# Kernel optimization log

Hardware: AMD Instinct MI355X
Metric: run time of the kernel (lower is better)

The kernel has to match this reference:

```python
import jax, jax.numpy as jnp
import numpy as np

B, T, C, H = 4, 2048, 1024, 16
HS = C // H  # head_size = 64


def setup_inputs() -> dict:
    key = jax.random.key(0)
    ks = jax.random.split(key, 12)
    s_in = C ** -0.5
    s_ff = (4 * C) ** -0.5
    return {
        "x": jax.random.normal(ks[0], (B, T, C), jnp.float32),
        "Wq": jax.random.normal(ks[1], (H, C, HS), jnp.float32) * s_in,
        "Wk": jax.random.normal(ks[2], (H, C, HS), jnp.float32) * s_in,
        "Wv": jax.random.normal(ks[3], (H, C, HS), jnp.float32) * s_in,
        "Wp": jax.random.normal(ks[4], (C, C), jnp.float32) * s_in,
        "bp": jnp.zeros((C,), jnp.float32),
        "W1": jax.random.normal(ks[5], (C, 4 * C), jnp.float32) * s_in,
        "b1": jnp.zeros((4 * C,), jnp.float32),
        "W2": jax.random.normal(ks[6], (4 * C, C), jnp.float32) * s_ff,
        "b2": jnp.zeros((C,), jnp.float32),
        "g1": jnp.ones((C,), jnp.float32),
        "be1": jnp.zeros((C,), jnp.float32),
        "g2": jnp.ones((C,), jnp.float32),
        "be2": jnp.zeros((C,), jnp.float32),
    }


def _layernorm(x, g, b, eps=1e-5):
    mu = jnp.mean(x, axis=-1, keepdims=True)
    var = jnp.var(x, axis=-1, keepdims=True)
    return (x - mu) * jax.lax.rsqrt(var + eps) * g + b


def reference(x, Wq, Wk, Wv, Wp, bp, W1, b1, W2, b2, g1, be1, g2, be2):
    # NOTE: residuals add to the post-LN tensor (faithful to the torch code),
    # and the attention scale uses C = n_embed, not head_size.
    x1 = _layernorm(x, g1, be1)                       # [B,T,C]
    q = jnp.einsum('btc,hcd->bhtd', x1, Wq)
    k = jnp.einsum('btc,hcd->bhtd', x1, Wk)
    v = jnp.einsum('btc,hcd->bhtd', x1, Wv)
    scores = jnp.einsum('bhtd,bhsd->bhts', q, k) * (C ** -0.5)
    causal = jnp.tril(jnp.ones((T, T), bool))
    scores = jnp.where(causal, scores, -jnp.inf)
    att = jax.nn.softmax(scores, axis=-1)             # [B,H,T,T]
    o = jnp.einsum('bhts,bhsd->bhtd', att, v)
    o = o.transpose(0, 2, 1, 3).reshape(B, T, C)      # concat heads
    x2 = x1 + o @ Wp + bp
    x3 = _layernorm(x2, g2, be2)
    ff = jax.nn.relu(x3 @ W1 + b1) @ W2 + b2
    return x3 + ff
```

## Files before the change

### kernel.cpp

```cpp
#include <hip/hip_runtime.h>
#include <cstdint>

typedef unsigned short u16;
typedef unsigned int u32;
typedef __bf16 bf16x8 __attribute__((ext_vector_type(8)));
typedef float f32x4 __attribute__((ext_vector_type(4)));

#define DEVINL __device__ __forceinline__

DEVINL float bf2f(u16 h) { union { u32 u; float f; } v; v.u = ((u32)h) << 16; return v.f; }
DEVINL u16 f2bf(float f) {
  union { __bf16 h; u16 u; } v;
  v.h = (__bf16)f;
  return v.u;
}

DEVINL float fexp2(float x) {
#if __has_builtin(__builtin_amdgcn_exp2f)
  return __builtin_amdgcn_exp2f(x);
#else
  return exp2f(x);
#endif
}

DEVINL void gld_lds16(const void* g, void* l) {
  __builtin_amdgcn_global_load_lds(
      (__attribute__((address_space(1))) void*)(g),
      (__attribute__((address_space(3))) void*)(l), 16, 0, 0);
}

__global__ __launch_bounds__(256) void kprep(
    const float* __restrict__ x, const float* __restrict__ Wq,
    const float* __restrict__ Wk, const float* __restrict__ Wv,
    const float* __restrict__ Wp, const float* __restrict__ W1,
    const float* __restrict__ W2, const float* __restrict__ g,
    const float* __restrict__ be, u16* __restrict__ x1,
    u16* __restrict__ wqkvT, u16* __restrict__ wpT,
    u16* __restrict__ w1T, u16* __restrict__ w2T) {
  int b = blockIdx.x;
  int t = threadIdx.x;
  if (b < 8192) {
    long row = b;
    float4 xv = *(const float4*)&x[row * 1024 + t * 4];
    float f0 = xv.x, f1 = xv.y, f2 = xv.z, f3 = xv.w;
    float s = f0 + f1 + f2 + f3;
    float s2 = f0 * f0 + f1 * f1 + f2 * f2 + f3 * f3;
#pragma unroll
    for (int off = 32; off >= 1; off >>= 1) {
      s += __shfl_xor(s, off);
      s2 += __shfl_xor(s2, off);
    }
    __shared__ float red[8];
    int w = t >> 6, l = t & 63;
    if (l == 0) { red[w] = s; red[4 + w] = s2; }
    __syncthreads();
    s = red[0] + red[1] + red[2] + red[3];
    s2 = red[4] + red[5] + red[6] + red[7];
    float mu = s * (1.0f / 1024.0f);
    float var = s2 * (1.0f / 1024.0f) - mu * mu;
    float rs = rsqrtf(var + 1e-5f);
    float4 gv = *(const float4*)&g[t * 4];
    float4 bv = *(const float4*)&be[t * 4];
    ushort4 ov;
    ov.x = f2bf((f0 - mu) * rs * gv.x + bv.x);
    ov.y = f2bf((f1 - mu) * rs * gv.y + bv.y);
    ov.z = f2bf((f2 - mu) * rs * gv.z + bv.z);
    ov.w = f2bf((f3 - mu) * rs * gv.w + bv.w);
    *(ushort4*)&x1[row * 1024 + t * 4] = ov;
    return;
  }
  int jb = b - 8192;
  const float* in;
  u16* out;
  int R, C, c0, r0;
  if (jb < 768) {
    int which = jb >> 8;
    int idx = jb & 255;
    int z = idx >> 4, y = idx & 15;
    const float* W = (which == 0) ? Wq : ((which == 1) ? Wk : Wv);
    in = W + (long)z * 65536;
    out = wqkvT + (long)which * 1048576 + (long)z * 65536;
    R = 1024; C = 64; c0 = 0; r0 = y * 64;
  } else if (jb < 1024) {
    int idx = jb - 768;
    in = Wp; out = wpT; R = 1024; C = 1024;
    c0 = (idx & 15) * 64; r0 = (idx >> 4) * 64;
  } else if (jb < 2048) {
    int idx = jb - 1024;
    in = W1; out = w1T; R = 1024; C = 4096;
    c0 = (idx & 63) * 64; r0 = (idx >> 6) * 64;
  } else {
    int idx = jb - 2048;
    in = W2; out = w2T; R = 4096; C = 1024;
    c0 = (idx & 15) * 64; r0 = (idx >> 4) * 64;
  }
  __shared__ __align__(16) u16 tile[64][80];
#pragma unroll
  for (int ph = 0; ph < 2; ++ph) {
    int ch = ph * 256 + t;
    int r = ch >> 3, cc = (ch & 7) * 8;
    const float* src = &in[(long)(r0 + r) * C + c0 + cc];
    float4 a = *(const float4*)src;
    float4 bb = *(const float4*)(src + 4);
    u16 tmp[8] = {f2bf(a.x), f2bf(a.y), f2bf(a.z), f2bf(a.w),
                  f2bf(bb.x), f2bf(bb.y), f2bf(bb.z), f2bf(bb.w)};
    *(uint4*)&tile[r][cc] = *(uint4*)tmp;
  }
  __syncthreads();
#pragma unroll
  for (int ph = 0; ph < 2; ++ph) {
    int ch = ph * 256 + t;
    int c = ch >> 3, rr = (ch & 7) * 8;
    u16 tmp[8];
#pragma unroll
    for (int i = 0; i < 8; ++i) tmp[i] = tile[rr + i][c];
    *(uint4*)&out[(long)(c0 + c) * R + r0 + rr] = *(uint4*)tmp;
  }
}

__global__ __launch_bounds__(256) void kln_b(const u16* __restrict__ x,
                                             const float* __restrict__ g,
                                             const float* __restrict__ be,
                                             u16* __restrict__ y) {
  long row = blockIdx.x;
  int t = threadIdx.x;
  ushort4 xv = *(const ushort4*)&x[row * 1024 + t * 4];
  float f0 = bf2f(xv.x), f1 = bf2f(xv.y), f2 = bf2f(xv.z), f3 = bf2f(xv.w);
  float s = f0 + f1 + f2 + f3;
  float s2 = f0 * f0 + f1 * f1 + f2 * f2 + f3 * f3;
#pragma unroll
  for (int off = 32; off >= 1; off >>= 1) {
    s += __shfl_xor(s, off);
    s2 += __shfl_xor(s2, off);
  }
  __shared__ float red[8];
  int w = t >> 6, l = t & 63;
  if (l == 0) { red[w] = s; red[4 + w] = s2; }
  __syncthreads();
  s = red[0] + red[1] + red[2] + red[3];
  s2 = red[4] + red[5] + red[6] + red[7];
  float mu = s * (1.0f / 1024.0f);
  float var = s2 * (1.0f / 1024.0f) - mu * mu;
  float rs = rsqrtf(var + 1e-5f);
  float4 gv = *(const float4*)&g[t * 4];
  float4 bv = *(const float4*)&be[t * 4];
  ushort4 ov;
  ov.x = f2bf((f0 - mu) * rs * gv.x + bv.x);
  ov.y = f2bf((f1 - mu) * rs * gv.y + bv.y);
  ov.z = f2bf((f2 - mu) * rs * gv.z + bv.z);
  ov.w = f2bf((f3 - mu) * rs * gv.w + bv.w);
  *(ushort4*)&y[row * 1024 + t * 4] = ov;
}

template <int EPI, int OF32>
__global__ __launch_bounds__(256) void kgemm(const u16* __restrict__ A,
                                             const u16* __restrict__ BT, int K,
                                             const float* __restrict__ bias,
                                             const u16* __restrict__ resid,
                                             void* __restrict__ outv, int ldc,
                                             u16* __restrict__ vout) {
  __shared__ __align__(16) u16 sA[128 * 64];
  __shared__ __align__(16) u16 sB[128 * 64];
  int tid = threadIdx.x;
  int l = tid & 63, wv = tid >> 6;
  int wm = (wv >> 1) * 64, wn = (wv & 1) * 64;
  int flat = blockIdx.y * gridDim.x + blockIdx.x;
  int cpx = (gridDim.x * gridDim.y) >> 3;
  int lg = (flat & 7) * cpx + (flat >> 3);
  int bx = lg % gridDim.x, by = lg / gridDim.x;
  long m0 = (long)by * 128, n0 = (long)bx * 128;
  const u16* Ab = A + m0 * K;
  const u16* Bb = BT + n0 * K;
  f32x4 acc[4][4] = {};

  for (int k0 = 0; k0 < K; k0 += 64) {
    __syncthreads();
#pragma unroll
    for (int it = 0; it < 4; ++it) {
      int c = it * 256 + tid;
      int r = c >> 3;
      int k8 = (c & 7) ^ (r & 7);
      gld_lds16(Ab + (long)r * K + k0 + k8 * 8, &sA[c * 8]);
    }
#pragma unroll
    for (int it = 0; it < 4; ++it) {
      int c = it * 256 + tid;
      int r = c >> 3;
      int k8 = (c & 7) ^ (r & 7);
      gld_lds16(Bb + (long)r * K + k0 + k8 * 8, &sB[c * 8]);
    }
    __syncthreads();
#pragma unroll
    for (int kk = 0; kk < 2; ++kk) {
      int k8 = kk * 4 + (l >> 4);
      bf16x8 af[4], bfr[4];
#pragma unroll
      for (int mi = 0; mi < 4; ++mi) {
        int r = wm + mi * 16 + (l & 15);
        af[mi] = *(const bf16x8*)&sA[(r * 8 + (k8 ^ (r & 7))) * 8];
      }
#pragma unroll
      for (int ni = 0; ni < 4; ++ni) {
        int r = wn + ni * 16 + (l & 15);
        bfr[ni] = *(const bf16x8*)&sB[(r * 8 + (k8 ^ (r & 7))) * 8];
      }
#pragma unroll
      for (int mi = 0; mi < 4; ++mi)
#pragma unroll
        for (int ni = 0; ni < 4; ++ni)
          acc[mi][ni] =
              __builtin_amdgcn_mfma_f32_16x16x32_bf16(af[mi], bfr[ni], acc[mi][ni], 0, 0, 0);
    }
  }
#pragma unroll
  for (int mi = 0; mi < 4; ++mi) {
#pragma unroll
    for (int ni = 0; ni < 4; ++ni) {
#pragma unroll
      for (int j = 0; j < 4; ++j) {
        long row = m0 + wm + mi * 16 + (l >> 4) * 4 + j;
        long col = n0 + wn + ni * 16 + (l & 15);
        float v = acc[mi][ni][j];
        if constexpr (EPI == 0) {
          long tn = col >> 10, jj = col & 1023;
          long hh = jj >> 6, dd = jj & 63;
          long bb = row >> 11, tt = row & 2047;
          if (tn == 0) {
            v *= 0.045084220027780106f;
            ((u16*)outv)[(((bb)*16 + hh) * 2048 + tt) * 64 + dd] = f2bf(v);
          } else if (tn == 1) {
            ((u16*)outv)[(((4 + bb) * 16 + hh) * 2048 + tt) * 64 + dd] = f2bf(v);
          } else {
            vout[((bb * 16 + hh) * 64 + dd) * 2048 + tt] = f2bf(v);
          }
        } else {
          v += bias[col];
          if constexpr (EPI == 2) v = fmaxf(v, 0.0f);
          if constexpr (EPI == 1) v += bf2f(resid[row * ldc + col]);
          if constexpr (OF32) ((float*)outv)[row * ldc + col] = v;
          else ((u16*)outv)[row * ldc + col] = f2bf(v);
        }
      }
    }
  }
}

__global__ __launch_bounds__(256) void kattn(const u16* __restrict__ q,
                                             const u16* __restrict__ kmat,
                                             const u16* __restrict__ vt,
                                             u16* __restrict__ o) {
  __shared__ __align__(16) u16 Ks[64 * 64];
  __shared__ __align__(16) u16 Vs[64 * 64];
  __shared__ __align__(16) u16 Ps[4 * 32 * 64];
  int bh = blockIdx.x;
  int qi = (gridDim.y - 1) - blockIdx.y;
  int tid = threadIdx.x, w = tid >> 6, l = tid & 63;
  long bQ = (long)bh * 2048 * 64;
  int qrow0 = qi * 128 + w * 32;
  const float NEGINF = -__builtin_inff();

  bf16x8 qf[2][2];
#pragma unroll
  for (int mi = 0; mi < 2; ++mi)
#pragma unroll
    for (int kk = 0; kk < 2; ++kk) {
      int tt = qrow0 + mi * 16 + (l & 15);
      int kd = kk * 32 + (l >> 4) * 8;
      qf[mi][kk] = *(const bf16x8*)&q[bQ + (long)tt * 64 + kd];
    }
  f32x4 ao[2][4] = {};
  float mr[2] = {NEGINF, NEGINF}, lr[2] = {0.f, 0.f};

  u16* Pw = &Ps[w * 2048];
  int g = l >> 4;
  int njt = qi * 2 + 2;
  for (int jt = 0; jt < njt; ++jt) {
    int s0 = jt * 64;
    bool skip = (s0 > qrow0 + 31);
    bool need_mask = (s0 + 63 > qrow0);
    __syncthreads();
#pragma unroll
    for (int it = 0; it < 2; ++it) {
      int c = it * 256 + tid;
      int r = c >> 3;
      int k8 = (c & 7) ^ (r & 7);
      gld_lds16(&kmat[bQ + (long)(s0 + r) * 64 + k8 * 8], &Ks[c * 8]);
    }
#pragma unroll
    for (int it = 0; it < 2; ++it) {
      int c = it * 256 + tid;
      int r = c >> 3;
      int s8 = (c & 7) ^ (r & 7);
      gld_lds16(&vt[bQ + (long)r * 2048 + s0 + s8 * 8], &Vs[c * 8]);
    }
    __syncthreads();
    if (skip) continue;
    f32x4 sc[2][4] = {};
#pragma unroll
    for (int kk = 0; kk < 2; ++kk) {
      int k8 = kk * 4 + g;
      bf16x8 kf[4];
#pragma unroll
      for (int ni = 0; ni < 4; ++ni) {
        int r = ni * 16 + (l & 15);
        kf[ni] = *(const bf16x8*)&Ks[(r * 8 + (k8 ^ (r & 7))) * 8];
      }
#pragma unroll
      for (int mi = 0; mi < 2; ++mi)
#pragma unroll
        for (int ni = 0; ni < 4; ++ni)
          sc[mi][ni] =
              __builtin_amdgcn_mfma_f32_16x16x32_bf16(kf[ni], qf[mi][kk], sc[mi][ni], 0, 0, 0);
    }
#pragma unroll
    for (int mi = 0; mi < 2; ++mi) {
      float rmax = NEGINF;
      if (need_mask) {
        int tg = qrow0 + mi * 16 + (l & 15);
#pragma unroll
        for (int ni = 0; ni < 4; ++ni)
#pragma unroll
          for (int j = 0; j < 4; ++j) {
            int sg = s0 + ni * 16 + g * 4 + j;
            float vv = sc[mi][ni][j];
            vv = (sg <= tg) ? vv : NEGINF;
            sc[mi][ni][j] = vv;
            rmax = fmaxf(rmax, vv);
          }
      } else {
#pragma unroll
        for (int ni = 0; ni < 4; ++ni)
#pragma unroll
          for (int j = 0; j < 4; ++j) rmax = fmaxf(rmax, sc[mi][ni][j]);
      }
      rmax = fmaxf(rmax, __shfl_xor(rmax, 16));
      rmax = fmaxf(rmax, __shfl_xor(rmax, 32));
      if (!__all(rmax <= mr[mi] + 11.5f)) {
        float mnew = fmaxf(mr[mi], rmax);
        float alpha = fexp2(mr[mi] - mnew);
        mr[mi] = mnew;
        lr[mi] *= alpha;
#pragma unroll
        for (int j = 0; j < 4; ++j) {
          float at = __shfl(alpha, g * 4 + j);
#pragma unroll
          for (int nd = 0; nd < 4; ++nd) ao[mi][nd][j] *= at;
        }
      }
      float rsum = 0.f;
#pragma unroll
      for (int ni = 0; ni < 4; ++ni)
#pragma unroll
        for (int j = 0; j < 4; ++j) {
          float p = fexp2(sc[mi][ni][j] - mr[mi]);
          sc[mi][ni][j] = p;
          rsum += p;
        }
      rsum += __shfl_xor(rsum, 16);
      rsum += __shfl_xor(rsum, 32);
      lr[mi] += rsum;
    }
#pragma unroll
    for (int mi = 0; mi < 2; ++mi) {
      int r = mi * 16 + (l & 15);
#pragma unroll
      for (int ni = 0; ni < 4; ++ni) {
        int cc0 = ni * 16 + g * 4;
        int addr = (r * 8 + ((cc0 >> 3) ^ (r & 7))) * 8 + (cc0 & 7);
        u16 h4[4] = {f2bf(sc[mi][ni][0]), f2bf(sc[mi][ni][1]),
                     f2bf(sc[mi][ni][2]), f2bf(sc[mi][ni][3])};
        *(uint2*)&Pw[addr] = *(uint2*)h4;
      }
    }
#pragma unroll
    for (int kk = 0; kk < 2; ++kk) {
      int s8 = kk * 4 + g;
      bf16x8 pf[2], vf[4];
#pragma unroll
      for (int mi = 0; mi < 2; ++mi) {
        int r = mi * 16 + (l & 15);
        pf[mi] = *(const bf16x8*)&Pw[(r * 8 + (s8 ^ (r & 7))) * 8];
      }
#pragma unroll
      for (int nd = 0; nd < 4; ++nd) {
        int r = nd * 16 + (l & 15);
        vf[nd] = *(const bf16x8*)&Vs[(r * 8 + (s8 ^ (r & 7))) * 8];
      }
#pragma unroll
      for (int mi = 0; mi < 2; ++mi)
#pragma unroll
        for (int nd = 0; nd < 4; ++nd)
          ao[mi][nd] =
              __builtin_amdgcn_mfma_f32_16x16x32_bf16(pf[mi], vf[nd], ao[mi][nd], 0, 0, 0);
    }
  }
  int b = bh >> 4, h = bh & 15;
#pragma unroll
  for (int mi = 0; mi < 2; ++mi) {
#pragma unroll
    for (int j = 0; j < 4; ++j) {
      float lrt = __shfl(lr[mi], g * 4 + j);
      float rinv = 1.0f / lrt;
#pragma unroll
      for (int nd = 0; nd < 4; ++nd) {
        int tt = qrow0 + mi * 16 + g * 4 + j;
        int dd = nd * 16 + (l & 15);
        o[((long)(b * 2048 + tt)) * 1024 + h * 64 + dd] = f2bf(ao[mi][nd][j] * rinv);
      }
    }
  }
}

extern "C" void kernel_launch(void* const* d_in, const int* in_sizes, int n_in,
                              void* d_out, int out_size, void* d_ws, size_t ws_size,
                              hipStream_t stream) {
  const float* x = (const float*)d_in[0];
  const float* Wq = (const float*)d_in[1];
  const float* Wk = (const float*)d_in[2];
  const float* Wv = (const float*)d_in[3];
  const float* Wp = (const float*)d_in[4];
  const float* bp = (const float*)d_in[5];
  const float* W1 = (const float*)d_in[6];
  const float* b1 = (const float*)d_in[7];
  const float* W2 = (const float*)d_in[8];
  const float* b2 = (const float*)d_in[9];
  const float* g1 = (const float*)d_in[10];
  const float* be1 = (const float*)d_in[11];
  const float* g2 = (const float*)d_in[12];
  const float* be2 = (const float*)d_in[13];

  u16* ws = (u16*)d_ws;
  u16* wqkvT = ws;
  u16* wpT = wqkvT + 3145728;
  u16* w1T = wpT + 1048576;
  u16* w2T = w1T + 4194304;
  u16* qb = w2T + 4194304;
  u16* kb = qb + 8388608;
  u16* vb = kb + 8388608;
  u16* vtb = vb + 8388608;
  u16* ob = vtb + 8388608;
  u16* x1 = ob + 8388608;
  float* outp = (float*)d_out;
  u16* x2 = vb;
  u16* x3 = ob;
  u16* hb = qb;

  kprep<<<11264, 256, 0, stream>>>(x, Wq, Wk, Wv, Wp, W1, W2, g1, be1,
                                   x1, wqkvT, wpT, w1T, w2T);

  kgemm<0, 0><<<dim3(24, 64), 256, 0, stream>>>(x1, wqkvT, 1024, nullptr, nullptr, qb, 0, vtb);
  kattn<<<dim3(64, 16), 256, 0, stream>>>(qb, kb, vtb, ob);
  kgemm<1, 0><<<dim3(8, 64), 256, 0, stream>>>(ob, wpT, 1024, bp, x1, x2, 1024, nullptr);
  kln_b<<<8192, 256, 0, stream>>>(x2, g2, be2, x3);
  kgemm<2, 0><<<dim3(32, 64), 256, 0, stream>>>(x3, w1T, 1024, b1, nullptr, hb, 4096, nullptr);
  kgemm<1, 1><<<dim3(8, 64), 256, 0, stream>>>(hb, w2T, 4096, b2, x3, outp, 1024, nullptr);
}
```

Baseline: 389.3 us.

## Add 256x256-tile 8-wave pipelined GEMM for FFN up-projection

Adds a new 512-thread GEMM kernel with 256x256 output tiles, a double-buffered LDS pipeline that interleaves staged global-to-LDS loads with MFMA phases, XOR-swizzled shared memory, s_setprio around the MFMA blocks, and a grouped block-index remap for L2 locality. It replaces the generic kgemm for the x3@W1+b1 ReLU matmul. The larger tiles give more data reuse per LDS byte and the pipelining is meant to hide load latency. In exchange it uses 128KB of LDS per block and a large accumulator register footprint, and it is hardcoded to the ReLU epilogue and to K being a multiple of 64.

```diff
diff --git a/kernel.cpp b/kernel.cpp
--- a/kernel.cpp
+++ b/kernel.cpp
@@ -245,6 +245,147 @@
   }
 }
 
+#define KG8_READB()                                                          \
+  _Pragma("unroll") for (int ni = 0; ni < 4; ++ni)                           \
+      _Pragma("unroll") for (int kk = 0; kk < 2; ++kk) {                     \
+    int r = wc * 64 + ni * 16 + (l & 15);                                    \
+    int s = (kk * 4 + (l >> 4)) ^ (r & 7);                                   \
+    bfr[ni][kk] = *(const bf16x8*)&sB[cur][(r * 8 + s) * 8];                 \
+  }
+#define KG8_PHASE2(qq)                                                       \
+  {                                                                          \
+    bf16x8 afr[2][2];                                                        \
+    _Pragma("unroll") for (int mi = 0; mi < 2; ++mi)                         \
+        _Pragma("unroll") for (int kk = 0; kk < 2; ++kk) {                   \
+      int r = wr * 128 + (qq)*32 + mi * 16 + (l & 15);                       \
+      int s = (kk * 4 + (l >> 4)) ^ (r & 7);                                 \
+      afr[mi][kk] = *(const bf16x8*)&sA[cur][(r * 8 + s) * 8];               \
+    }                                                                        \
+    __builtin_amdgcn_s_barrier();                                            \
+    asm volatile("s_waitcnt lgkmcnt(0)" ::: "memory");                       \
+    __builtin_amdgcn_sched_barrier(0);                                       \
+    __builtin_amdgcn_s_setprio(1);                                           \
+    _Pragma("unroll") for (int kk = 0; kk < 2; ++kk)                         \
+        _Pragma("unroll") for (int mi = 0; mi < 2; ++mi)                     \
+            _Pragma("unroll") for (int ni = 0; ni < 4; ++ni)                 \
+                acc[(qq)*2 + mi][ni] =                                       \
+                    __builtin_amdgcn_mfma_f32_16x16x32_bf16(                 \
+                        afr[mi][kk], bfr[ni][kk], acc[(qq)*2 + mi][ni],      \
+                        0, 0, 0);                                            \
+    __builtin_amdgcn_s_setprio(0);                                           \
+    __builtin_amdgcn_sched_barrier(0);                                       \
+  }
+
+__global__ __launch_bounds__(512, 2) void kgemm8(const u16* __restrict__ A,
+                                                 const u16* __restrict__ BT,
+                                                 int K,
+                                                 const float* __restrict__ bias,
+                                                 u16* __restrict__ out, int ldc) {
+  __shared__ __align__(16) u16 sA[2][256 * 64];
+  __shared__ __align__(16) u16 sB[2][256 * 64];
+  int tid = threadIdx.x;
+  int w = tid >> 6, l = tid & 63;
+  int wr = w >> 2, wc = w & 3;
+  int flat = blockIdx.y * gridDim.x + blockIdx.x;
+  int cpx = (gridDim.x * gridDim.y) >> 3;
+  int lg = (flat & 7) * cpx + (flat >> 3);
+  int bx = lg % gridDim.x, by = lg / gridDim.x;
+  long m0 = (long)by * 256, n0 = (long)bx * 256;
+  const u16* Ab = A + m0 * K;
+  const u16* Bb = BT + n0 * K;
+  int nt = K >> 6;
+  f32x4 acc[8][4] = {};
+
+  auto stageA = [&](int b, int t, int p) {
+    int ri = tid >> 3;
+    int r = (ri < 32) ? (p * 32 + ri) : (128 + p * 32 + (ri - 32));
+    int s = tid & 7;
+    int k8 = s ^ (r & 7);
+    int chunk = (ri < 32) ? (p * 256 + tid) : (1024 + p * 256 + (tid - 256));
+    gld_lds16(Ab + (long)r * K + t * 64 + k8 * 8, &sA[b][chunk * 8]);
+  };
+  auto stageB = [&](int b, int t, int p) {
+    int r = p * 64 + (tid >> 3);
+    int s = tid & 7;
+    int k8 = s ^ (r & 7);
+    gld_lds16(Bb + (long)r * K + t * 64 + k8 * 8, &sB[b][(p * 512 + tid) * 8]);
+  };
+
+#pragma unroll
+  for (int p = 0; p < 4; ++p) { stageA(0, 0, p); stageB(0, 0, p); }
+#pragma unroll
+  for (int p = 0; p < 3; ++p) { stageA(1, 1, p); stageB(1, 1, p); }
+  asm volatile("s_waitcnt vmcnt(6)" ::: "memory");
+  __builtin_amdgcn_s_barrier();
+
+  for (int t = 0; t + 2 < nt; ++t) {
+    const int cur = t & 1;
+    const int nxt = cur ^ 1;
+    bf16x8 bfr[4][2];
+    stageA(nxt, t + 1, 3);
+    stageB(nxt, t + 1, 3);
+    KG8_READB();
+    KG8_PHASE2(0);
+    __builtin_amdgcn_s_barrier();
+    stageA(cur, t + 2, 0);
+    stageB(cur, t + 2, 0);
+    KG8_PHASE2(1);
+    __builtin_amdgcn_s_barrier();
+    stageA(cur, t + 2, 1);
+    stageB(cur, t + 2, 1);
+    KG8_PHASE2(2);
+    __builtin_amdgcn_s_barrier();
+    stageA(cur, t + 2, 2);
+    stageB(cur, t + 2, 2);
+    KG8_PHASE2(3);
+    asm volatile("s_waitcnt vmcnt(6)" ::: "memory");
+    __builtin_amdgcn_s_barrier();
+  }
+  {
+    const int cur = (nt - 2) & 1;
+    const int nxt = cur ^ 1;
+    stageA(nxt, nt - 1, 3);
+    stageB(nxt, nt - 1, 3);
+    bf16x8 bfr[4][2];
+    KG8_READB();
+    KG8_PHASE2(0);
+    __builtin_amdgcn_s_barrier();
+    KG8_PHASE2(1);
+    __builtin_amdgcn_s_barrier();
+    KG8_PHASE2(2);
+    __builtin_amdgcn_s_barrier();
+    KG8_PHASE2(3);
+    asm volatile("s_waitcnt vmcnt(0)" ::: "memory");
+    __builtin_amdgcn_s_barrier();
+  }
+  {
+    const int cur = (nt - 1) & 1;
+    bf16x8 bfr[4][2];
+    KG8_READB();
+    KG8_PHASE2(0);
+    __builtin_amdgcn_s_barrier();
+    KG8_PHASE2(1);
+    __builtin_amdgcn_s_barrier();
+    KG8_PHASE2(2);
+    __builtin_amdgcn_s_barrier();
+    KG8_PHASE2(3);
+  }
+#pragma unroll
+  for (int m8 = 0; m8 < 8; ++m8) {
+#pragma unroll
+    for (int ni = 0; ni < 4; ++ni) {
+#pragma unroll
+      for (int j = 0; j < 4; ++j) {
+        long row = m0 + wr * 128 + m8 * 16 + (l >> 4) * 4 + j;
+        long col = n0 + wc * 64 + ni * 16 + (l & 15);
+        float v = acc[m8][ni][j] + bias[col];
+        v = fmaxf(v, 0.0f);
+        out[row * (long)ldc + col] = f2bf(v);
+      }
+    }
+  }
+}
+
 __global__ __launch_bounds__(256) void kattn(const u16* __restrict__ q,
                                              const u16* __restrict__ kmat,
                                              const u16* __restrict__ vt,
@@ -452,6 +593,6 @@
   kattn<<<dim3(64, 16), 256, 0, stream>>>(qb, kb, vtb, ob);
   kgemm<1, 0><<<dim3(8, 64), 256, 0, stream>>>(ob, wpT, 1024, bp, x1, x2, 1024, nullptr);
   kln_b<<<8192, 256, 0, stream>>>(x2, g2, be2, x3);
-  kgemm<2, 0><<<dim3(32, 64), 256, 0, stream>>>(x3, w1T, 1024, b1, nullptr, hb, 4096, nullptr);
+  kgemm8<<<dim3(16, 32), 512, 0, stream>>>(x3, w1T, 1024, b1, hb, 4096);
   kgemm<1, 1><<<dim3(8, 64), 256, 0, stream>>>(hb, w2T, 4096, b2, x3, outp, 1024, nullptr);
 }
```

New measurement: 396.7 us. No clear change (+1.9%).
